# Kernel optimization log

Measured on AMD Instinct MI355X. Metric: run time of the kernel, lower is better.

Reference implementation:

```python
import jax, jax.numpy as jnp
import numpy as np

N_NODES = 25000
N_EDGES = 100000
N_GRAPHS = 1000
DIM = 64
NUM_FEAT = 14
EDGE_FEAT = 4
HIDDEN_EDGE = 128
NUM_OUT = 1
NUM_CONV_STEPS = 3
SET2SET_STEPS = 3
NEG_SLOPE = 0.01


def leaky_relu(x):
    return jnp.where(x > 0, x, NEG_SLOPE * x)


def setup_inputs() -> dict:
    key = jax.random.key(0)
    ks = jax.random.split(key, 24)
    s = lambda fan_in: 1.0 / np.sqrt(fan_in)
    inp = {
        "x": jax.random.normal(ks[0], (N_NODES, NUM_FEAT), dtype=jnp.float32),
        "edge_index": jax.random.randint(ks[1], (2, N_EDGES), 0, N_NODES),
        "edge_attr": jax.random.uniform(ks[2], (N_EDGES, EDGE_FEAT), dtype=jnp.float32),
        "batch": jnp.sort(jax.random.randint(ks[3], (N_NODES,), 0, N_GRAPHS)),
        # lin0
        "lin0_w": jax.random.normal(ks[4], (DIM, NUM_FEAT), dtype=jnp.float32) * s(NUM_FEAT),
        "lin0_b": jnp.zeros((DIM,), dtype=jnp.float32),
        # edge-weight MLP: Linear(4,128) -> LeakyReLU -> Linear(128, DIM*DIM)
        "net_w1": jax.random.normal(ks[5], (HIDDEN_EDGE, EDGE_FEAT), dtype=jnp.float32) * s(EDGE_FEAT),
        "net_b1": jnp.zeros((HIDDEN_EDGE,), dtype=jnp.float32),
        "net_w2": jax.random.normal(ks[6], (DIM * DIM, HIDDEN_EDGE), dtype=jnp.float32) * s(HIDDEN_EDGE),
        "net_b2": jnp.zeros((DIM * DIM,), dtype=jnp.float32),
        # NNConv root weight + bias
        "conv_root": jax.random.normal(ks[7], (DIM, DIM), dtype=jnp.float32) * s(DIM),
        "conv_bias": jnp.zeros((DIM,), dtype=jnp.float32),
        # GRU (single layer), torch gate order r,z,n
        "gru_w_ih": jax.random.normal(ks[8], (3 * DIM, DIM), dtype=jnp.float32) * s(DIM),
        "gru_w_hh": jax.random.normal(ks[9], (3 * DIM, DIM), dtype=jnp.float32) * s(DIM),
        "gru_b_ih": jnp.zeros((3 * DIM,), dtype=jnp.float32),
        "gru_b_hh": jnp.zeros((3 * DIM,), dtype=jnp.float32),
        # Set2Set LSTM: input 2*DIM -> hidden DIM, torch gate order i,f,g,o
        "lstm_w_ih": jax.random.normal(ks[10], (4 * DIM, 2 * DIM), dtype=jnp.float32) * s(2 * DIM),
        "lstm_w_hh": jax.random.normal(ks[11], (4 * DIM, DIM), dtype=jnp.float32) * s(DIM),
        "lstm_b_ih": jnp.zeros((4 * DIM,), dtype=jnp.float32),
        "lstm_b_hh": jnp.zeros((4 * DIM,), dtype=jnp.float32),
        # final linear on [B, 2*DIM]
        "lin_w": jax.random.normal(ks[12], (NUM_OUT, 2 * DIM), dtype=jnp.float32) * s(2 * DIM),
        "lin_b": jnp.zeros((NUM_OUT,), dtype=jnp.float32),
    }
    return inp


def _forward(x, edge_index, edge_attr, batch,
             lin0_w, lin0_b, net_w1, net_b1, net_w2, net_b2,
             conv_root, conv_bias, gru_w_ih, gru_w_hh, gru_b_ih, gru_b_hh,
             lstm_w_ih, lstm_w_hh, lstm_b_ih, lstm_b_hh, lin_w, lin_b):
    src, dst = edge_index[0], edge_index[1]

    out = leaky_relu(x @ lin0_w.T + lin0_b)          # [N, DIM]
    h = out                                          # GRU hidden [N, DIM]

    # edge_attr is constant across conv steps -> dynamic weights computed once
    W_e = (leaky_relu(edge_attr @ net_w1.T + net_b1) @ net_w2.T + net_b2)
    W_e = W_e.reshape(N_EDGES, DIM, DIM)             # [E, DIM, DIM]

    deg = jax.ops.segment_sum(jnp.ones((N_EDGES,), dtype=x.dtype), dst,
                              num_segments=N_NODES)
    inv_deg = jnp.where(deg > 0, 1.0 / jnp.maximum(deg, 1.0), 0.0)[:, None]

    for _ in range(NUM_CONV_STEPS):
        # NNConv: gather -> per-edge matmul -> scatter-mean, plus root term
        msg = jnp.einsum('ed,edo->eo', out[src], W_e)                 # [E, DIM]
        aggr = jax.ops.segment_sum(msg, dst, num_segments=N_NODES) * inv_deg
        m = leaky_relu(aggr + out @ conv_root + conv_bias)
        # single-step GRU (torch equations, gate order r,z,n)
        gi = m @ gru_w_ih.T + gru_b_ih
        gh = h @ gru_w_hh.T + gru_b_hh
        i_r, i_z, i_n = jnp.split(gi, 3, axis=-1)
        h_r, h_z, h_n = jnp.split(gh, 3, axis=-1)
        r = jax.nn.sigmoid(i_r + h_r)
        z = jax.nn.sigmoid(i_z + h_z)
        n = jnp.tanh(i_n + r * h_n)
        h = (1.0 - z) * n + z * h
        out = h

    # Set2Set pooling (processing_steps=3)
    q_star = jnp.zeros((N_GRAPHS, 2 * DIM), dtype=x.dtype)
    hl = jnp.zeros((N_GRAPHS, DIM), dtype=x.dtype)
    cl = jnp.zeros((N_GRAPHS, DIM), dtype=x.dtype)
    for _ in range(SET2SET_STEPS):
        gates = q_star @ lstm_w_ih.T + lstm_b_ih + hl @ lstm_w_hh.T + lstm_b_hh
        gi, gf, gg, go = jnp.split(gates, 4, axis=-1)
        cl = jax.nn.sigmoid(gf) * cl + jax.nn.sigmoid(gi) * jnp.tanh(gg)
        hl = jax.nn.sigmoid(go) * jnp.tanh(cl)
        q = hl                                                         # [B, DIM]
        e = jnp.sum(out * q[batch], axis=-1)                           # [N]
        e_max = jax.ops.segment_max(e, batch, num_segments=N_GRAPHS)
        e_exp = jnp.exp(e - e_max[batch])
        denom = jax.ops.segment_sum(e_exp, batch, num_segments=N_GRAPHS)
        a = e_exp / denom[batch]                                       # segment softmax
        r_read = jax.ops.segment_sum(a[:, None] * out, batch,
                                     num_segments=N_GRAPHS)            # [B, DIM]
        q_star = jnp.concatenate([q, r_read], axis=-1)

    return q_star @ lin_w.T + lin_b                                    # [B, NUM_OUT]


def reference(x, edge_index, edge_attr, batch,
              lin0_w, lin0_b, net_w1, net_b1, net_w2, net_b2,
              conv_root, conv_bias, gru_w_ih, gru_w_hh, gru_b_ih, gru_b_hh,
              lstm_w_ih, lstm_w_hh, lstm_b_ih, lstm_b_hh, lin_w, lin_b):
    return _forward(x, edge_index, edge_attr, batch,
                    lin0_w, lin0_b, net_w1, net_b1, net_w2, net_b2,
                    conv_root, conv_bias, gru_w_ih, gru_w_hh, gru_b_ih, gru_b_hh,
                    lstm_w_ih, lstm_w_hh, lstm_b_ih, lstm_b_hh, lin_w, lin_b)
```

## Files before the change

kernel.cpp:

```cpp
#include <hip/hip_runtime.h>
#include <math.h>

#define N_NODES_C  25000
#define N_EDGES_C  100000
#define N_GRAPHS_C 1000
#define EPB 128

typedef __attribute__((ext_vector_type(8))) _Float16 f16x8;
typedef __attribute__((ext_vector_type(2))) _Float16 f16x2;
typedef __attribute__((ext_vector_type(4))) float   f32x4;

__device__ __forceinline__ float lrelu(float x) { return x > 0.f ? x : 0.01f * x; }
__device__ __forceinline__ float sigm(float x)  { return 1.f / (1.f + __expf(-x)); }
__device__ __forceinline__ f32x4 MFH(f16x8 a, f16x8 b, f32x4 c) {
  return __builtin_amdgcn_mfma_f32_16x16x32_f16(a, b, c, 0, 0, 0);
}

__global__ __launch_bounds__(256) void lin0_kernel(const float* __restrict__ x,
                            const float* __restrict__ w, const float* __restrict__ b,
                            float* __restrict__ nodeF) {
  __shared__ float ws[64 * 15];
  __shared__ float bs[64];
  __shared__ float xr[4][16];
  const int tid = threadIdx.x;
  for (int i = tid; i < 896; i += 256) { int o = i / 14, j = i % 14; ws[o * 15 + j] = w[i]; }
  if (tid < 64) bs[tid] = b[tid];
  const int nl = tid >> 6, o = tid & 63;
  const int n = blockIdx.x * 4 + nl;
  if (o < 14 && n < N_NODES_C) xr[nl][o] = x[n * 14 + o];
  __syncthreads();
  if (n < N_NODES_C) {
    float s = bs[o];
#pragma unroll
    for (int j = 0; j < 14; ++j) s += xr[nl][j] * ws[o * 15 + j];
    nodeF[n * 64 + o] = lrelu(s);
  }
}

__global__ void deg_kernel(const int* __restrict__ ei, float* __restrict__ deg) {
  int e = blockIdx.x * blockDim.x + threadIdx.x;
  if (e < N_EDGES_C) atomicAdd(&deg[ei[N_EDGES_C + e]], 1.f);
}

__global__ void invdeg_kernel(float* __restrict__ deg) {
  int n = blockIdx.x * blockDim.x + threadIdx.x;
  if (n < N_NODES_C) { float v = deg[n]; deg[n] = v > 0.f ? 1.f / v : 0.f; }
}

__global__ void goff_kernel(const int* __restrict__ batch, int* __restrict__ goff) {
  int g = blockIdx.x * blockDim.x + threadIdx.x;
  if (g > N_GRAPHS_C) return;
  int lo = 0, hi = N_NODES_C;
  while (lo < hi) { int mid = (lo + hi) >> 1; if (batch[mid] < g) lo = mid + 1; else hi = mid; }
  goff[g] = lo;
}

__global__ void prep_gru_kernel(const float* __restrict__ conv_root,
                                const float* __restrict__ w_ih, const float* __restrict__ w_hh,
                                _Float16* __restrict__ Rtp,
                                _Float16* __restrict__ Wip, _Float16* __restrict__ Whp) {
  int i = blockIdx.x * 256 + threadIdx.x;
  if (i < 12288) {
    int j = i & 7, lane = (i >> 3) & 63, kc = (i >> 9) & 1, t = i >> 10;
    int o = t * 16 + (lane & 15), d = kc * 32 + (lane >> 4) * 8 + j;
    if (i < 4096) Rtp[i] = (_Float16)conv_root[d * 64 + o];
    Wip[i] = (_Float16)w_ih[o * 64 + d];
    Whp[i] = (_Float16)w_hh[o * 64 + d];
  }
}

__global__ __launch_bounds__(256) void prep_w2_kernel(
    const float* __restrict__ net_w2, const float* __restrict__ net_b2,
    _Float16* __restrict__ Wp, _Float16* __restrict__ B2p) {
  int i = blockIdx.x * 256 + threadIdx.x;
  {
    int j = i & 7, lane = (i >> 3) & 63, q = (i >> 9) & 3, p = (i >> 11) & 1;
    int oh = (i >> 12) & 1, d = i >> 13;
    int kci = q >> 1, ob = q & 1;
    int col = lane & 15, kg = lane >> 4;
    int o = oh * 32 + ob * 16 + col, h = (p * 2 + kci) * 32 + kg * 8 + j;
    Wp[i] = (_Float16)net_w2[((size_t)d * 64 + o) * 128 + h];
  }
  if (i < 4096) {
    int j = i & 7, lane = (i >> 3) & 63, kc2 = (i >> 9) & 1, ob = (i >> 10) & 1, oh = (i >> 11) & 1;
    int col = lane & 15, kg = lane >> 4;
    int o = oh * 32 + ob * 16 + col, d = kc2 * 32 + kg * 8 + j;
    B2p[i] = (_Float16)net_b2[d * 64 + o];
  }
}

__global__ __launch_bounds__(256, 4) void msg_kernel(
    const float* __restrict__ nodef,
    const int*   __restrict__ ei,
    const float* __restrict__ eattr,
    const float* __restrict__ net_w1,
    const float* __restrict__ net_b1,
    const _Float16* __restrict__ Wp,
    const _Float16* __restrict__ B2p,
    float* __restrict__ aggr)
{
  __shared__ _Float16 xsT[EPB * 64];
  __shared__ float    w1s[128 * 5];

  const int tid = threadIdx.x;
  const int e0 = blockIdx.x * EPB;

  if (tid < 128) {
    float4 wv = *(const float4*)(net_w1 + tid * 4);
    w1s[tid * 5 + 0] = wv.x; w1s[tid * 5 + 1] = wv.y;
    w1s[tid * 5 + 2] = wv.z; w1s[tid * 5 + 3] = wv.w;
    w1s[tid * 5 + 4] = net_b1[tid];
  }
  {
    const int e = tid >> 1, dh = (tid & 1) * 32;
    int ge = e0 + e;
    const int esw = (e & 7) << 3;
#pragma unroll
    for (int jb = 0; jb < 4; ++jb) {
      int d = dh + jb * 8;
      float4 v0, v1;
      if (ge < N_EDGES_C) {
        const float4* nf4 = (const float4*)(nodef + (size_t)ei[ge] * 64 + d);
        v0 = nf4[0]; v1 = nf4[1];
      } else {
        v0 = make_float4(0.f, 0.f, 0.f, 0.f); v1 = v0;
      }
      f16x8 pk;
      pk[0] = (_Float16)v0.x; pk[1] = (_Float16)v0.y; pk[2] = (_Float16)v0.z; pk[3] = (_Float16)v0.w;
      pk[4] = (_Float16)v1.x; pk[5] = (_Float16)v1.y; pk[6] = (_Float16)v1.z; pk[7] = (_Float16)v1.w;
      *(f16x8*)&xsT[e * 64 + (d ^ esw)] = pk;
    }
  }

  const int lane = tid & 63, wv = tid >> 6;
  const int e0w = (wv & 1) * 64;
  const int oh  = wv >> 1;
  const int col = lane & 15;
  const int kg  = lane >> 4;
  const int swz = (col & 7) << 3;

  __syncthreads();

  f32x4 acc[4][2];
#pragma unroll
  for (int eb = 0; eb < 4; ++eb) { acc[eb][0] = 0.f; acc[eb][1] = 0.f; }
#pragma unroll
  for (int ob = 0; ob < 2; ++ob)
#pragma unroll
    for (int kc2 = 0; kc2 < 2; ++kc2) {
      f16x8 b2f = *(const f16x8*)(B2p + oh * 2048 + ob * 1024 + kc2 * 512 + lane * 8);
#pragma unroll
      for (int eb = 0; eb < 4; ++eb) {
        f16x8 xf = *(const f16x8*)&xsT[(e0w + eb * 16 + col) * 64 + ((kc2 * 32 + kg * 8) ^ swz)];
        acc[eb][ob] = MFH(xf, b2f, acc[eb][ob]);
      }
    }

  const _Float16* wp_base = Wp + oh * 4096 + lane * 8;
#pragma unroll 1
  for (int p = 0; p < 2; ++p) {
    f16x8 Af[4][2];
    {
      float4 at[4];
#pragma unroll
      for (int eb = 0; eb < 4; ++eb) {
        int ge = e0 + e0w + eb * 16 + col;
        at[eb] = (ge < N_EDGES_C) ? *(const float4*)(eattr + (size_t)ge * 4)
                                  : make_float4(0.f, 0.f, 0.f, 0.f);
      }
#pragma unroll
      for (int kci = 0; kci < 2; ++kci) {
        float4 wr[8]; float wb[8];
#pragma unroll
        for (int j = 0; j < 8; ++j) {
          int hq = (p * 2 + kci) * 32 + kg * 8 + j;
          wr[j] = *(const float4*)&w1s[hq * 5];
          wb[j] = w1s[hq * 5 + 4];
        }
#pragma unroll
        for (int eb = 0; eb < 4; ++eb) {
          f16x8 F;
#pragma unroll
          for (int j = 0; j < 8; ++j) {
            float a = wb[j] + at[eb].x * wr[j].x + at[eb].y * wr[j].y
                            + at[eb].z * wr[j].z + at[eb].w * wr[j].w;
            F[j] = (_Float16)lrelu(a);
          }
          Af[eb][kci] = F;
        }
      }
    }

    const _Float16* wp_p = wp_base + p * 2048;
    f16x8 Bb[2][4];
#define LOADB(BUF, dd)                                                   \
  {                                                                      \
    const _Float16* b_ = wp_p + (size_t)(dd) * 8192;                     \
    BUF[0] = *(const f16x8*)(b_);                                        \
    BUF[1] = *(const f16x8*)(b_ + 512);                                  \
    BUF[2] = *(const f16x8*)(b_ + 1024);                                 \
    BUF[3] = *(const f16x8*)(b_ + 1536);                                 \
  }
    LOADB(Bb[0], 0);
#pragma unroll 1
    for (int d8 = 0; d8 < 64; d8 += 8) {
      union { f16x8 v; unsigned u[4]; } XV[4];
#pragma unroll
      for (int eb = 0; eb < 4; ++eb)
        XV[eb].v = *(const f16x8*)&xsT[(e0w + eb * 16 + col) * 64 + (d8 ^ swz)];
#pragma unroll
      for (int j = 0; j < 8; ++j) {
        int d = d8 + j;
        if (d < 63) LOADB(Bb[(j + 1) & 1], d + 1);
        const f16x8* B = Bb[j & 1];
#pragma unroll
        for (int eb = 0; eb < 4; ++eb) {
          unsigned dw = XV[eb].u[j >> 1];
          unsigned xd = __builtin_amdgcn_perm(dw, dw, (j & 1) ? 0x03020302u : 0x01000100u);
          f16x2 x2; { union { unsigned u; f16x2 h; } c; c.u = xd; x2 = c.h; }
#pragma unroll
          for (int kci = 0; kci < 2; ++kci) {
            union { f16x8 v; f16x2 p[4]; } af, Uu;
            af.v = Af[eb][kci];
#pragma unroll
            for (int q = 0; q < 4; ++q) Uu.p[q] = af.p[q] * x2;
            acc[eb][0] = MFH(Uu.v, B[kci * 2 + 0], acc[eb][0]);
            acc[eb][1] = MFH(Uu.v, B[kci * 2 + 1], acc[eb][1]);
          }
        }
      }
    }
#undef LOADB
  }

  const int o0w = oh * 32;
#pragma unroll
  for (int eb = 0; eb < 4; ++eb) {
#pragma unroll
    for (int r = 0; r < 4; ++r) {
      int e = e0w + eb * 16 + kg * 4 + r;
      int ge = e0 + e;
      if (ge < N_EDGES_C) {
        int dn = ei[N_EDGES_C + ge];
        atomicAdd(&aggr[(size_t)dn * 64 + o0w + col],      acc[eb][0][r]);
        atomicAdd(&aggr[(size_t)dn * 64 + o0w + 16 + col], acc[eb][1][r]);
      }
    }
  }
}

__global__ __launch_bounds__(256) void node_update_kernel(
    float* __restrict__ aggr, const float* __restrict__ invdeg,
    const _Float16* __restrict__ Rtp, const _Float16* __restrict__ Wip,
    const _Float16* __restrict__ Whp,
    const float* __restrict__ conv_bias,
    const float* __restrict__ b_ih, const float* __restrict__ b_hh,
    float* __restrict__ nodeF)
{
  __shared__ _Float16 ms[4][16 * 64];

  const int tid = threadIdx.x, lane = tid & 63, wv = tid >> 6;
  const int col = lane & 15, kg = lane >> 4;
  const int nwb = blockIdx.x * 64 + wv * 16;

  int arow = nwb + col; if (arow >= N_NODES_C) arow = N_NODES_C - 1;
  f16x8 nf[2];
#pragma unroll
  for (int kc = 0; kc < 2; ++kc) {
    f32x4 v0 = *(const f32x4*)(nodeF + (size_t)arow * 64 + kc * 32 + kg * 8);
    f32x4 v1 = *(const f32x4*)(nodeF + (size_t)arow * 64 + kc * 32 + kg * 8 + 4);
    f16x8 F;
#pragma unroll
    for (int j = 0; j < 4; ++j) { F[j] = (_Float16)v0[j]; F[4 + j] = (_Float16)v1[j]; }
    nf[kc] = F;
  }

  f32x4 racc[4];
#pragma unroll
  for (int t = 0; t < 4; ++t) racc[t] = conv_bias[t * 16 + col];
#pragma unroll
  for (int t = 0; t < 4; ++t)
#pragma unroll
    for (int kc = 0; kc < 2; ++kc)
      racc[t] = MFH(nf[kc], *(const f16x8*)(Rtp + t * 1024 + kc * 512 + lane * 8), racc[t]);

  float invd[4]; int nrow[4];
#pragma unroll
  for (int r = 0; r < 4; ++r) {
    int nn = nwb + kg * 4 + r; nrow[r] = nn;
    invd[r] = (nn < N_NODES_C) ? invdeg[nn] : 0.f;
  }
#pragma unroll
  for (int t = 0; t < 4; ++t) {
#pragma unroll
    for (int r = 0; r < 4; ++r) {
      int nn = nrow[r];
      float ag = 0.f;
      if (nn < N_NODES_C) {
        size_t idx = (size_t)nn * 64 + t * 16 + col;
        ag = aggr[idx];
        aggr[idx] = 0.f;
      }
      float mval = lrelu(ag * invd[r] + racc[t][r]);
      int nl = kg * 4 + r;
      int dsw = (t * 16 + col) ^ ((nl & 7) << 3);
      ms[wv][nl * 64 + dsw] = (_Float16)mval;
    }
  }
  __syncthreads();

  f16x8 ma[2];
#pragma unroll
  for (int kc = 0; kc < 2; ++kc)
    ma[kc] = *(const f16x8*)&ms[wv][col * 64 + ((kc * 32 + kg * 8) ^ ((col & 7) << 3))];

  f32x4 gi[12], gh[12];
#pragma unroll
  for (int t = 0; t < 12; ++t) { gi[t] = b_ih[t * 16 + col]; gh[t] = b_hh[t * 16 + col]; }
#pragma unroll
  for (int t = 0; t < 12; ++t)
#pragma unroll
    for (int kc = 0; kc < 2; ++kc) {
      gi[t] = MFH(ma[kc], *(const f16x8*)(Wip + t * 1024 + kc * 512 + lane * 8), gi[t]);
      gh[t] = MFH(nf[kc], *(const f16x8*)(Whp + t * 1024 + kc * 512 + lane * 8), gh[t]);
    }

#pragma unroll
  for (int t = 0; t < 4; ++t) {
#pragma unroll
    for (int r = 0; r < 4; ++r) {
      int nn = nrow[r];
      if (nn >= N_NODES_C) continue;
      size_t idx = (size_t)nn * 64 + t * 16 + col;
      float hv = nodeF[idx];
      float rr = sigm(gi[t][r] + gh[t][r]);
      float zz = sigm(gi[t + 4][r] + gh[t + 4][r]);
      float nv = tanhf(gi[t + 8][r] + rr * gh[t + 8][r]);
      nodeF[idx] = (1.f - zz) * nv + zz * hv;
    }
  }
}

__global__ __launch_bounds__(64) void set2set_kernel(
    const float* __restrict__ nodeF, const int* __restrict__ goff,
    const float* __restrict__ w_ih, const float* __restrict__ w_hh,
    const float* __restrict__ b_ih, const float* __restrict__ b_hh,
    const float* __restrict__ lw, const float* __restrict__ lb,
    float* __restrict__ ebuf, float* __restrict__ dout)
{
  const int g = blockIdx.x, t = threadIdx.x;
  __shared__ float qs[128], hs[64];
  float hl = 0.f, cl = 0.f;
  qs[t] = 0.f; qs[64 + t] = 0.f;
  const int s0 = goff[g], s1 = goff[g + 1];

  for (int step = 0; step < 3; ++step) {
    hs[t] = hl;
    __syncthreads();
    float gv[4];
#pragma unroll
    for (int k = 0; k < 4; ++k) {
      float s = b_ih[k * 64 + t] + b_hh[k * 64 + t];
      const float4* wi4 = (const float4*)(w_ih + (k * 64 + t) * 128);
#pragma unroll 8
      for (int j = 0; j < 32; ++j) {
        float4 w = wi4[j];
        s += qs[4 * j] * w.x + qs[4 * j + 1] * w.y + qs[4 * j + 2] * w.z + qs[4 * j + 3] * w.w;
      }
      const float4* wh4 = (const float4*)(w_hh + (k * 64 + t) * 64);
#pragma unroll 8
      for (int j = 0; j < 16; ++j) {
        float4 w = wh4[j];
        s += hs[4 * j] * w.x + hs[4 * j + 1] * w.y + hs[4 * j + 2] * w.z + hs[4 * j + 3] * w.w;
      }
      gv[k] = s;
    }
    cl = sigm(gv[1]) * cl + sigm(gv[0]) * tanhf(gv[2]);
    hl = sigm(gv[3]) * tanhf(cl);
    const float qv = hl;

    float emax = -3.0e38f;
    for (int n = s0; n < s1; ++n) {
      float p = nodeF[n * 64 + t] * qv;
#pragma unroll
      for (int off = 32; off > 0; off >>= 1) p += __shfl_down(p, off);
      float en = __shfl(p, 0);
      if (t == 0) ebuf[n] = en;
      emax = fmaxf(emax, en);
    }
    __syncthreads();
    float lsum = 0.f;
    for (int n = s0 + t; n < s1; n += 64) {
      float ex = __expf(ebuf[n] - emax);
      ebuf[n] = ex;
      lsum += ex;
    }
#pragma unroll
    for (int off = 32; off > 0; off >>= 1) lsum += __shfl_down(lsum, off);
    float denom = __shfl(lsum, 0);
    __syncthreads();
    float r = 0.f;
    for (int n = s0; n < s1; ++n) r += ebuf[n] * nodeF[n * 64 + t];
    if (s1 > s0) r /= denom;
    qs[t] = qv; qs[64 + t] = r;
  }
  __syncthreads();
  float s = qs[t] * lw[t] + qs[64 + t] * lw[64 + t];
#pragma unroll
  for (int off = 32; off > 0; off >>= 1) s += __shfl_down(s, off);
  if (t == 0) dout[g] = s + lb[0];
}

extern "C" void kernel_launch(void* const* d_in, const int* in_sizes, int n_in,
                              void* d_out, int out_size, void* d_ws, size_t ws_size,
                              hipStream_t stream) {
  const float* x         = (const float*)d_in[0];
  const int*   ei        = (const int*)  d_in[1];
  const float* eattr     = (const float*)d_in[2];
  const int*   batch     = (const int*)  d_in[3];
  const float* lin0_w    = (const float*)d_in[4];
  const float* lin0_b    = (const float*)d_in[5];
  const float* net_w1    = (const float*)d_in[6];
  const float* net_b1    = (const float*)d_in[7];
  const float* net_w2    = (const float*)d_in[8];
  const float* net_b2    = (const float*)d_in[9];
  const float* conv_root = (const float*)d_in[10];
  const float* conv_bias = (const float*)d_in[11];
  const float* gru_w_ih  = (const float*)d_in[12];
  const float* gru_w_hh  = (const float*)d_in[13];
  const float* gru_b_ih  = (const float*)d_in[14];
  const float* gru_b_hh  = (const float*)d_in[15];
  const float* lstm_w_ih = (const float*)d_in[16];
  const float* lstm_w_hh = (const float*)d_in[17];
  const float* lstm_b_ih = (const float*)d_in[18];
  const float* lstm_b_hh = (const float*)d_in[19];
  const float* lin_w     = (const float*)d_in[20];
  const float* lin_b     = (const float*)d_in[21];

  float* ws    = (float*)d_ws;
  float* nodeF = ws;
  float* aggr  = nodeF + 1600000;
  float* deg   = aggr + 1600000;
  float* ebuf  = deg + 25000;
  int*   goff  = (int*)(ebuf + 25000);
  _Float16* Rtp = (_Float16*)(goff + 1024);
  _Float16* Wip = Rtp + 4096;
  _Float16* Whp = Wip + 12288;
  _Float16* Wp  = Whp + 12288;
  _Float16* B2p = Wp + 524288;

  hipMemsetAsync(deg, 0, 25000 * sizeof(float), stream);
  hipMemsetAsync(aggr, 0, 1600000 * sizeof(float), stream);

  lin0_kernel<<<(N_NODES_C + 3) / 4, 256, 0, stream>>>(x, lin0_w, lin0_b, nodeF);
  deg_kernel<<<(N_EDGES_C + 255) / 256, 256, 0, stream>>>(ei, deg);
  invdeg_kernel<<<(N_NODES_C + 255) / 256, 256, 0, stream>>>(deg);
  goff_kernel<<<(N_GRAPHS_C + 256) / 256, 256, 0, stream>>>(batch, goff);
  prep_gru_kernel<<<48, 256, 0, stream>>>(conv_root, gru_w_ih, gru_w_hh, Rtp, Wip, Whp);
  prep_w2_kernel<<<2048, 256, 0, stream>>>(net_w2, net_b2, Wp, B2p);

  for (int step = 0; step < 3; ++step) {
    msg_kernel<<<(N_EDGES_C + EPB - 1) / EPB, 256, 0, stream>>>(
        nodeF, ei, eattr, net_w1, net_b1, Wp, B2p, aggr);
    node_update_kernel<<<(N_NODES_C + 63) / 64, 256, 0, stream>>>(
        aggr, deg, Rtp, Wip, Whp, conv_bias, gru_b_ih, gru_b_hh, nodeF);
  }

  set2set_kernel<<<N_GRAPHS_C, 64, 0, stream>>>(
      nodeF, goff, lstm_w_ih, lstm_w_hh, lstm_b_ih, lstm_b_hh, lin_w, lin_b, ebuf, (float*)d_out);
}
```

Measured before the change: 602.2 us.

## Restructure msg_kernel to 128-thread blocks with each wave covering all 128 edges

Reorganizes the fused edge-network message kernel so each block has two waves, each owning 32 output columns for all 128 edges, rather than four waves splitting edges and outputs. Each wave now loads half the Wp fragments per d step, and each B fragment is reused across eight edge tiles instead of four, which halves global/L2 traffic for the large expanded weight. The hidden dimension is processed in four passes of 32 instead of two of 64. The cost is more accumulator registers per thread (16 f32x4) and fewer waves per block, which may lower occupancy and latency hiding.

```diff
diff --git a/kernel.cpp b/kernel.cpp
--- a/kernel.cpp
+++ b/kernel.cpp
@@ -89,7 +89,7 @@
   }
 }
 
-__global__ __launch_bounds__(256, 4) void msg_kernel(
+__global__ __launch_bounds__(128, 2) void msg_kernel(
     const float* __restrict__ nodef,
     const int*   __restrict__ ei,
     const float* __restrict__ eattr,
@@ -105,19 +105,19 @@
   const int tid = threadIdx.x;
   const int e0 = blockIdx.x * EPB;
 
-  if (tid < 128) {
+  {
     float4 wv = *(const float4*)(net_w1 + tid * 4);
     w1s[tid * 5 + 0] = wv.x; w1s[tid * 5 + 1] = wv.y;
     w1s[tid * 5 + 2] = wv.z; w1s[tid * 5 + 3] = wv.w;
     w1s[tid * 5 + 4] = net_b1[tid];
   }
   {
-    const int e = tid >> 1, dh = (tid & 1) * 32;
-    int ge = e0 + e;
+    const int e = tid;
+    const int ge = e0 + e;
     const int esw = (e & 7) << 3;
 #pragma unroll
-    for (int jb = 0; jb < 4; ++jb) {
-      int d = dh + jb * 8;
+    for (int jb = 0; jb < 8; ++jb) {
+      int d = jb * 8;
       float4 v0, v1;
       if (ge < N_EDGES_C) {
         const float4* nf4 = (const float4*)(nodef + (size_t)ei[ge] * 64 + d);
@@ -132,101 +132,86 @@
     }
   }
 
-  const int lane = tid & 63, wv = tid >> 6;
-  const int e0w = (wv & 1) * 64;
-  const int oh  = wv >> 1;
-  const int col = lane & 15;
-  const int kg  = lane >> 4;
-  const int swz = (col & 7) << 3;
+  const int lane = tid & 63;
+  const int oh   = tid >> 6;
+  const int col  = lane & 15;
+  const int kg   = lane >> 4;
+  const int swz  = (col & 7) << 3;
 
   __syncthreads();
 
-  f32x4 acc[4][2];
-#pragma unroll
-  for (int eb = 0; eb < 4; ++eb) { acc[eb][0] = 0.f; acc[eb][1] = 0.f; }
+  f32x4 acc[8][2];
+#pragma unroll
+  for (int eb = 0; eb < 8; ++eb) { acc[eb][0] = 0.f; acc[eb][1] = 0.f; }
 #pragma unroll
   for (int ob = 0; ob < 2; ++ob)
 #pragma unroll
     for (int kc2 = 0; kc2 < 2; ++kc2) {
       f16x8 b2f = *(const f16x8*)(B2p + oh * 2048 + ob * 1024 + kc2 * 512 + lane * 8);
 #pragma unroll
-      for (int eb = 0; eb < 4; ++eb) {
-        f16x8 xf = *(const f16x8*)&xsT[(e0w + eb * 16 + col) * 64 + ((kc2 * 32 + kg * 8) ^ swz)];
+      for (int eb = 0; eb < 8; ++eb) {
+        f16x8 xf = *(const f16x8*)&xsT[(eb * 16 + col) * 64 + ((kc2 * 32 + kg * 8) ^ swz)];
         acc[eb][ob] = MFH(xf, b2f, acc[eb][ob]);
       }
     }
 
-  const _Float16* wp_base = Wp + oh * 4096 + lane * 8;
 #pragma unroll 1
-  for (int p = 0; p < 2; ++p) {
-    f16x8 Af[4][2];
+  for (int p = 0; p < 4; ++p) {
+    f16x8 Af[8];
     {
-      float4 at[4];
-#pragma unroll
-      for (int eb = 0; eb < 4; ++eb) {
-        int ge = e0 + e0w + eb * 16 + col;
-        at[eb] = (ge < N_EDGES_C) ? *(const float4*)(eattr + (size_t)ge * 4)
-                                  : make_float4(0.f, 0.f, 0.f, 0.f);
-      }
-#pragma unroll
-      for (int kci = 0; kci < 2; ++kci) {
-        float4 wr[8]; float wb[8];
+      float4 wr[8]; float wb[8];
+#pragma unroll
+      for (int j = 0; j < 8; ++j) {
+        int hq = p * 32 + kg * 8 + j;
+        wr[j] = *(const float4*)&w1s[hq * 5];
+        wb[j] = w1s[hq * 5 + 4];
+      }
+#pragma unroll
+      for (int eb = 0; eb < 8; ++eb) {
+        int ge = e0 + eb * 16 + col;
+        float4 at = (ge < N_EDGES_C) ? *(const float4*)(eattr + (size_t)ge * 4)
+                                     : make_float4(0.f, 0.f, 0.f, 0.f);
+        f16x8 F;
 #pragma unroll
         for (int j = 0; j < 8; ++j) {
-          int hq = (p * 2 + kci) * 32 + kg * 8 + j;
-          wr[j] = *(const float4*)&w1s[hq * 5];
-          wb[j] = w1s[hq * 5 + 4];
+          float a = wb[j] + at.x * wr[j].x + at.y * wr[j].y + at.z * wr[j].z + at.w * wr[j].w;
+          F[j] = (_Float16)lrelu(a);
         }
-#pragma unroll
-        for (int eb = 0; eb < 4; ++eb) {
-          f16x8 F;
-#pragma unroll
-          for (int j = 0; j < 8; ++j) {
-            float a = wb[j] + at[eb].x * wr[j].x + at[eb].y * wr[j].y
-                            + at[eb].z * wr[j].z + at[eb].w * wr[j].w;
-            F[j] = (_Float16)lrelu(a);
-          }
-          Af[eb][kci] = F;
-        }
-      }
-    }
-
-    const _Float16* wp_p = wp_base + p * 2048;
-    f16x8 Bb[2][4];
+        Af[eb] = F;
+      }
+    }
+
+    const _Float16* wp_p = Wp + (((oh * 2 + (p >> 1)) * 4 + (p & 1) * 2) * 64 + lane) * 8;
+    f16x8 Bb[2][2];
 #define LOADB(BUF, dd)                                                   \
   {                                                                      \
     const _Float16* b_ = wp_p + (size_t)(dd) * 8192;                     \
     BUF[0] = *(const f16x8*)(b_);                                        \
     BUF[1] = *(const f16x8*)(b_ + 512);                                  \
-    BUF[2] = *(const f16x8*)(b_ + 1024);                                 \
-    BUF[3] = *(const f16x8*)(b_ + 1536);                                 \
   }
     LOADB(Bb[0], 0);
 #pragma unroll 1
     for (int d8 = 0; d8 < 64; d8 += 8) {
-      union { f16x8 v; unsigned u[4]; } XV[4];
-#pragma unroll
-      for (int eb = 0; eb < 4; ++eb)
-        XV[eb].v = *(const f16x8*)&xsT[(e0w + eb * 16 + col) * 64 + (d8 ^ swz)];
+      union { f16x8 v; unsigned u[4]; } XV[8];
+#pragma unroll
+      for (int eb = 0; eb < 8; ++eb)
+        XV[eb].v = *(const f16x8*)&xsT[(eb * 16 + col) * 64 + (d8 ^ swz)];
 #pragma unroll
       for (int j = 0; j < 8; ++j) {
         int d = d8 + j;
         if (d < 63) LOADB(Bb[(j + 1) & 1], d + 1);
         const f16x8* B = Bb[j & 1];
 #pragma unroll
-        for (int eb = 0; eb < 4; ++eb) {
+        for (int eb = 0; eb < 8; ++eb) {
           unsigned dw = XV[eb].u[j >> 1];
           unsigned xd = __builtin_amdgcn_perm(dw, dw, (j & 1) ? 0x03020302u : 0x01000100u);
           f16x2 x2; { union { unsigned u; f16x2 h; } c; c.u = xd; x2 = c.h; }
-#pragma unroll
-          for (int kci = 0; kci < 2; ++kci) {
-            union { f16x8 v; f16x2 p[4]; } af, Uu;
-            af.v = Af[eb][kci];
-#pragma unroll
-            for (int q = 0; q < 4; ++q) Uu.p[q] = af.p[q] * x2;
-            acc[eb][0] = MFH(Uu.v, B[kci * 2 + 0], acc[eb][0]);
-            acc[eb][1] = MFH(Uu.v, B[kci * 2 + 1], acc[eb][1]);
-          }
+          union { f16x8 v; f16x2 pp[4]; } af, Uu;
+          af.v = Af[eb];
+#pragma unroll
+          for (int q = 0; q < 4; ++q) Uu.pp[q] = af.pp[q] * x2;
+          acc[eb][0] = MFH(Uu.v, B[0], acc[eb][0]);
+          acc[eb][1] = MFH(Uu.v, B[1], acc[eb][1]);
         }
       }
     }
@@ -235,10 +220,10 @@
 
   const int o0w = oh * 32;
 #pragma unroll
-  for (int eb = 0; eb < 4; ++eb) {
+  for (int eb = 0; eb < 8; ++eb) {
 #pragma unroll
     for (int r = 0; r < 4; ++r) {
-      int e = e0w + eb * 16 + kg * 4 + r;
+      int e = eb * 16 + kg * 4 + r;
       int ge = e0 + e;
       if (ge < N_EDGES_C) {
         int dn = ei[N_EDGES_C + ge];
@@ -460,7 +445,7 @@
   prep_w2_kernel<<<2048, 256, 0, stream>>>(net_w2, net_b2, Wp, B2p);
 
   for (int step = 0; step < 3; ++step) {
-    msg_kernel<<<(N_EDGES_C + EPB - 1) / EPB, 256, 0, stream>>>(
+    msg_kernel<<<(N_EDGES_C + EPB - 1) / EPB, 128, 0, stream>>>(
         nodeF, ei, eattr, net_w1, net_b1, Wp, B2p, aggr);
     node_update_kernel<<<(N_NODES_C + 63) / 64, 256, 0, stream>>>(
         aggr, deg, Rtp, Wip, Whp, conv_bias, gru_b_ih, gru_b_hh, nodeF);
```

After: 632.7 us. 5.1% more time.

## Split edge-weight K loop into four passes with depth-3 B prefetch

Applied to the files above, without the earlier changes.

The fused edge-message MFMA loop now runs four passes over 32-wide hidden chunks instead of two passes over 64. Each pass keeps one A fragment per edge block and loads two B fragments per d step. B-weight loads are prefetched three steps ahead through a 4-slot register ring instead of double-buffered one step ahead. This cuts live registers per pass and hides more global-load latency, at the cost of rereading xsT and recomputing edge features in twice as many passes.

```diff
diff --git a/kernel.cpp b/kernel.cpp
--- a/kernel.cpp
+++ b/kernel.cpp
@@ -156,52 +156,41 @@
       }
     }
 
-  const _Float16* wp_base = Wp + oh * 4096 + lane * 8;
 #pragma unroll 1
-  for (int p = 0; p < 2; ++p) {
-    f16x8 Af[4][2];
+  for (int p = 0; p < 4; ++p) {
+    f16x8 Af[4];
     {
-      float4 at[4];
+      float4 wr[8]; float wb[8];
+#pragma unroll
+      for (int j = 0; j < 8; ++j) {
+        int hq = p * 32 + kg * 8 + j;
+        wr[j] = *(const float4*)&w1s[hq * 5];
+        wb[j] = w1s[hq * 5 + 4];
+      }
 #pragma unroll
       for (int eb = 0; eb < 4; ++eb) {
         int ge = e0 + e0w + eb * 16 + col;
-        at[eb] = (ge < N_EDGES_C) ? *(const float4*)(eattr + (size_t)ge * 4)
-                                  : make_float4(0.f, 0.f, 0.f, 0.f);
-      }
-#pragma unroll
-      for (int kci = 0; kci < 2; ++kci) {
-        float4 wr[8]; float wb[8];
+        float4 at = (ge < N_EDGES_C) ? *(const float4*)(eattr + (size_t)ge * 4)
+                                     : make_float4(0.f, 0.f, 0.f, 0.f);
+        f16x8 F;
 #pragma unroll
         for (int j = 0; j < 8; ++j) {
-          int hq = (p * 2 + kci) * 32 + kg * 8 + j;
-          wr[j] = *(const float4*)&w1s[hq * 5];
-          wb[j] = w1s[hq * 5 + 4];
+          float a = wb[j] + at.x * wr[j].x + at.y * wr[j].y + at.z * wr[j].z + at.w * wr[j].w;
+          F[j] = (_Float16)lrelu(a);
         }
-#pragma unroll
-        for (int eb = 0; eb < 4; ++eb) {
-          f16x8 F;
-#pragma unroll
-          for (int j = 0; j < 8; ++j) {
-            float a = wb[j] + at[eb].x * wr[j].x + at[eb].y * wr[j].y
-                            + at[eb].z * wr[j].z + at[eb].w * wr[j].w;
-            F[j] = (_Float16)lrelu(a);
-          }
-          Af[eb][kci] = F;
-        }
-      }
-    }
-
-    const _Float16* wp_p = wp_base + p * 2048;
-    f16x8 Bb[2][4];
+        Af[eb] = F;
+      }
+    }
+
+    const _Float16* wp_p = Wp + (((oh * 2 + (p >> 1)) * 4 + (p & 1) * 2) * 64 + lane) * 8;
+    f16x8 Bq[4][2];
 #define LOADB(BUF, dd)                                                   \
   {                                                                      \
     const _Float16* b_ = wp_p + (size_t)(dd) * 8192;                     \
     BUF[0] = *(const f16x8*)(b_);                                        \
     BUF[1] = *(const f16x8*)(b_ + 512);                                  \
-    BUF[2] = *(const f16x8*)(b_ + 1024);                                 \
-    BUF[3] = *(const f16x8*)(b_ + 1536);                                 \
-  }
-    LOADB(Bb[0], 0);
+  }
+    LOADB(Bq[0], 0); LOADB(Bq[1], 1); LOADB(Bq[2], 2);
 #pragma unroll 1
     for (int d8 = 0; d8 < 64; d8 += 8) {
       union { f16x8 v; unsigned u[4]; } XV[4];
@@ -211,22 +200,19 @@
 #pragma unroll
       for (int j = 0; j < 8; ++j) {
         int d = d8 + j;
-        if (d < 63) LOADB(Bb[(j + 1) & 1], d + 1);
-        const f16x8* B = Bb[j & 1];
+        if (d + 3 < 64) LOADB(Bq[(j + 3) & 3], d + 3);
+        const f16x8* B = Bq[j & 3];
 #pragma unroll
         for (int eb = 0; eb < 4; ++eb) {
           unsigned dw = XV[eb].u[j >> 1];
           unsigned xd = __builtin_amdgcn_perm(dw, dw, (j & 1) ? 0x03020302u : 0x01000100u);
           f16x2 x2; { union { unsigned u; f16x2 h; } c; c.u = xd; x2 = c.h; }
-#pragma unroll
-          for (int kci = 0; kci < 2; ++kci) {
-            union { f16x8 v; f16x2 p[4]; } af, Uu;
-            af.v = Af[eb][kci];
-#pragma unroll
-            for (int q = 0; q < 4; ++q) Uu.p[q] = af.p[q] * x2;
-            acc[eb][0] = MFH(Uu.v, B[kci * 2 + 0], acc[eb][0]);
-            acc[eb][1] = MFH(Uu.v, B[kci * 2 + 1], acc[eb][1]);
-          }
+          union { f16x8 v; f16x2 pp[4]; } af, Uu;
+          af.v = Af[eb];
+#pragma unroll
+          for (int q = 0; q < 4; ++q) Uu.pp[q] = af.pp[q] * x2;
+          acc[eb][0] = MFH(Uu.v, B[0], acc[eb][0]);
+          acc[eb][1] = MFH(Uu.v, B[1], acc[eb][1]);
         }
       }
     }
```

New measurement: 607.3 us. About the same (+0.9%).
